# Performance work log

Hardware: AMD Instinct MI355X
Metric: run time of the kernel (lower is better)

## Reference

```python
import jax, jax.numpy as jnp
import numpy as np

N_LAYER = 4
N_HEAD = 8
N_EMBD = 512
HEAD_SIZE = N_EMBD // N_HEAD
VOCAB = 32000
BLOCK = 2048
WINDOW = 64
N_GLOBAL = 16
N_RANDOM = 16
B = 2
T = 2048


def setup_inputs() -> dict:
    key = jax.random.key(0)
    ks = jax.random.split(key, 24)
    s = 0.02
    inp = {
        "tok_emb": jax.random.normal(ks[0], (VOCAB, N_EMBD), jnp.float32) * s,
        "pos_emb": jax.random.normal(ks[1], (BLOCK, N_EMBD), jnp.float32) * s,
        "Wq": jax.random.normal(ks[2], (N_LAYER, N_HEAD, N_EMBD, HEAD_SIZE), jnp.float32) * s,
        "Wk": jax.random.normal(ks[3], (N_LAYER, N_HEAD, N_EMBD, HEAD_SIZE), jnp.float32) * s,
        "Wv": jax.random.normal(ks[4], (N_LAYER, N_HEAD, N_EMBD, HEAD_SIZE), jnp.float32) * s,
        "Wproj": jax.random.normal(ks[5], (N_LAYER, N_EMBD, N_EMBD), jnp.float32) * s,
        "bproj": jnp.zeros((N_LAYER, N_EMBD), jnp.float32),
        "ln1_g": jnp.ones((N_LAYER, N_EMBD), jnp.float32),
        "ln1_b": jnp.zeros((N_LAYER, N_EMBD), jnp.float32),
        "ln2_g": jnp.ones((N_LAYER, N_EMBD), jnp.float32),
        "ln2_b": jnp.zeros((N_LAYER, N_EMBD), jnp.float32),
        "W1": jax.random.normal(ks[6], (N_LAYER, N_EMBD, 4 * N_EMBD), jnp.float32) * s,
        "b1": jnp.zeros((N_LAYER, 4 * N_EMBD), jnp.float32),
        "W2": jax.random.normal(ks[7], (N_LAYER, 4 * N_EMBD, N_EMBD), jnp.float32) * s,
        "b2": jnp.zeros((N_LAYER, N_EMBD), jnp.float32),
        "lnf_g": jnp.ones((N_EMBD,), jnp.float32),
        "lnf_b": jnp.zeros((N_EMBD,), jnp.float32),
        "Wout": jax.random.normal(ks[8], (N_EMBD, VOCAB), jnp.float32) * s,
        "bout": jnp.zeros((VOCAB,), jnp.float32),
        "input_tokens": jax.random.randint(ks[9], (B, T), 0, VOCAB, jnp.int32),
        "random_cols": jax.random.randint(ks[10], (N_LAYER, N_HEAD, T, N_RANDOM), 0, T, jnp.int32),
    }
    return inp


def _layernorm(x, g, b):
    mu = jnp.mean(x, axis=-1, keepdims=True)
    var = jnp.var(x, axis=-1, keepdims=True)
    return (x - mu) * jax.lax.rsqrt(var + 1e-5) * g + b


def _static_masks(t):
    rows = jnp.arange(t)[:, None]
    cols = jnp.arange(t)[None, :]
    causal = rows >= cols
    local = (cols >= rows - WINDOW + 1) & (cols <= rows)
    glob = (rows < N_GLOBAL) | (cols < N_GLOBAL)
    return local | glob, causal  # base [T,T], causal [T,T]


def _random_mask(rc):  # rc: [H, T, R] -> [H, T, T] bool
    h, t, r = rc.shape
    m = jnp.zeros((h, t, t), dtype=bool)
    hi = jnp.arange(h)[:, None, None]
    ri = jnp.arange(t)[None, :, None]
    return m.at[hi, ri, rc].set(True)


def _forward(tok_emb, pos_emb, Wq, Wk, Wv, Wproj, bproj, ln1_g, ln1_b, ln2_g, ln2_b,
             W1, b1, W2, b2, lnf_g, lnf_b, Wout, bout, input_tokens, random_cols):
    b, t = input_tokens.shape
    x = tok_emb[input_tokens] + pos_emb[:t]  # [B,T,C]
    base, causal = _static_masks(t)
    scale = HEAD_SIZE ** -0.5
    neg_inf = jnp.finfo(x.dtype).min
    for l in range(N_LAYER):
        xn = _layernorm(x, ln1_g[l], ln1_b[l])
        q = jnp.einsum('btc,hcd->bhtd', xn, Wq[l])
        k = jnp.einsum('btc,hcd->bhtd', xn, Wk[l])
        v = jnp.einsum('btc,hcd->bhtd', xn, Wv[l])
        w = jnp.einsum('bhtd,bhsd->bhts', q, k) * scale  # [B,H,T,T]
        final = (base[None] | _random_mask(random_cols[l])) & causal[None]  # [H,T,T]
        w = jnp.where(final[None], w, neg_inf)
        w = jax.nn.softmax(w, axis=-1)
        attn = jnp.einsum('bhts,bhsd->bhtd', w, v)  # [B,H,T,hs]
        attn = attn.transpose(0, 2, 1, 3).reshape(b, t, N_EMBD)
        x = x + attn @ Wproj[l] + bproj[l]
        xn = _layernorm(x, ln2_g[l], ln2_b[l])
        h = jax.nn.relu(xn @ W1[l] + b1[l])
        x = x + h @ W2[l] + b2[l]
    x = _layernorm(x, lnf_g, lnf_b)
    return x @ Wout + bout  # logits [B,T,V]


def reference(tok_emb, pos_emb, Wq, Wk, Wv, Wproj, bproj, ln1_g, ln1_b, ln2_g, ln2_b,
              W1, b1, W2, b2, lnf_g, lnf_b, Wout, bout, input_tokens, random_cols):
    return _forward(tok_emb, pos_emb, Wq, Wk, Wv, Wproj, bproj, ln1_g, ln1_b, ln2_g, ln2_b,
                    W1, b1, W2, b2, lnf_g, lnf_b, Wout, bout, input_tokens, random_cols)
```

## Files before the change

### kernel.cpp

```cpp
#include <hip/hip_runtime.h>
#include <hip/hip_bf16.h>

#define NLAYER 4
#define NHEAD 8
#define CEMB 512
#define HS 64
#define VOCAB_N 32000
#define SEQT 2048
#define BATCH_N 2
#define MROWS (BATCH_N * SEQT)
#define WIN 64
#define NGLOB 16
#define NRAND 16
#define QB 16
#define VTW 104
#define PSW 104

typedef __attribute__((ext_vector_type(8))) __bf16 bf16x8;
typedef __attribute__((ext_vector_type(4))) float f32x4;
typedef __attribute__((ext_vector_type(8))) unsigned short u16x8;

__device__ __forceinline__ unsigned short f2bf(float f) {
    unsigned u = __float_as_uint(f);
    u += 0x7fffu + ((u >> 16) & 1u);
    return (unsigned short)(u >> 16);
}
__device__ __forceinline__ float bf2f(unsigned short v) {
    return __uint_as_float((unsigned)v << 16);
}

__device__ __forceinline__ void stage16(const unsigned short* g, unsigned short* l) {
    __builtin_amdgcn_global_load_lds(
        (const __attribute__((address_space(1))) void*)g,
        (__attribute__((address_space(3))) void*)l, 16, 0, 0);
}

__global__ __launch_bounds__(256) void transpose_all_kernel(
    const float* __restrict__ Wq, const float* __restrict__ Wk,
    const float* __restrict__ Wv, const float* __restrict__ Wproj,
    const float* __restrict__ W1, const float* __restrict__ W2,
    const float* __restrict__ Wout,
    unsigned short* __restrict__ wqkvT, unsigned short* __restrict__ wprojT,
    unsigned short* __restrict__ w1T, unsigned short* __restrict__ w2T,
    unsigned short* __restrict__ woutT)
{
    __shared__ float tle[64][65];
    const int bid = blockIdx.x;
    const float* src; unsigned short* dst; int Ks, Ns, k0, n0;
    if (bid < 768) {
        const int tile = bid & 7, rest = bid >> 3;
        const int l = rest / 24, r2 = rest % 24;
        const int sel = r2 >> 3, h = r2 & 7;
        const float* W = (sel == 0) ? Wq : (sel == 1) ? Wk : Wv;
        src = W + (size_t)(l * 8 + h) * 512 * 64;
        dst = wqkvT + ((size_t)l * 1536 + sel * 512 + h * 64) * 512;
        Ks = 512; Ns = 64; k0 = tile * 64; n0 = 0;
    } else if (bid < 1024) {
        const int idx = bid - 768, l = idx >> 6, t6 = idx & 63;
        src = Wproj + (size_t)l * 512 * 512;
        dst = wprojT + (size_t)l * 512 * 512;
        Ks = 512; Ns = 512; k0 = (t6 >> 3) * 64; n0 = (t6 & 7) * 64;
    } else if (bid < 2048) {
        const int idx = bid - 1024, l = idx >> 8, t8 = idx & 255;
        src = W1 + (size_t)l * 512 * 2048;
        dst = w1T + (size_t)l * 2048 * 512;
        Ks = 512; Ns = 2048; k0 = (t8 >> 5) * 64; n0 = (t8 & 31) * 64;
    } else if (bid < 3072) {
        const int idx = bid - 2048, l = idx >> 8, t8 = idx & 255;
        src = W2 + (size_t)l * 2048 * 512;
        dst = w2T + (size_t)l * 512 * 2048;
        Ks = 2048; Ns = 512; k0 = (t8 >> 3) * 64; n0 = (t8 & 7) * 64;
    } else {
        const int idx = bid - 3072;
        src = Wout; dst = woutT;
        Ks = 512; Ns = 32000; k0 = (idx / 500) * 64; n0 = (idx % 500) * 64;
    }
    const int tid = threadIdx.x;
    #pragma unroll
    for (int i = 0; i < 16; ++i) {
        const int idx = tid + i * 256;
        const int r = idx >> 6, c = idx & 63;
        tle[r][c] = src[(size_t)(k0 + r) * Ns + n0 + c];
    }
    __syncthreads();
    #pragma unroll
    for (int i = 0; i < 16; ++i) {
        const int idx = tid + i * 256;
        const int c = idx >> 6, r = idx & 63;
        dst[(size_t)(n0 + c) * Ks + k0 + r] = f2bf(tle[r][c]);
    }
}

__global__ __launch_bounds__(256) void embed_kernel(
    const float* __restrict__ tok_emb, const float* __restrict__ pos_emb,
    const int* __restrict__ toks, float* __restrict__ x)
{
    int i = blockIdx.x * 256 + threadIdx.x;
    int m = i >> 7;
    int c = (i & 127) << 2;
    int tok = toks[m];
    const float4 a = *(const float4*)&tok_emb[(size_t)tok * CEMB + c];
    const float4 p = *(const float4*)&pos_emb[(size_t)(m & (SEQT - 1)) * CEMB + c];
    float4 o;
    o.x = a.x + p.x; o.y = a.y + p.y; o.z = a.z + p.z; o.w = a.w + p.w;
    *(float4*)&x[(size_t)m * CEMB + c] = o;
}

__global__ __launch_bounds__(256) void ln_kernel(
    const float* __restrict__ x, const float* __restrict__ g,
    const float* __restrict__ b, unsigned short* __restrict__ out)
{
    const int wave = threadIdx.x >> 6, lane = threadIdx.x & 63;
    const int m = blockIdx.x * 4 + wave;
    const float* row = x + (size_t)m * CEMB;
    const float4 v0 = *(const float4*)&row[lane * 8];
    const float4 v1 = *(const float4*)&row[lane * 8 + 4];
    float s  = v0.x + v0.y + v0.z + v0.w + v1.x + v1.y + v1.z + v1.w;
    float s2 = v0.x*v0.x + v0.y*v0.y + v0.z*v0.z + v0.w*v0.w
             + v1.x*v1.x + v1.y*v1.y + v1.z*v1.z + v1.w*v1.w;
    #pragma unroll
    for (int off = 32; off > 0; off >>= 1) {
        s  += __shfl_xor(s, off);
        s2 += __shfl_xor(s2, off);
    }
    const float mu  = s * (1.f / CEMB);
    const float var = s2 * (1.f / CEMB) - mu * mu;
    const float rs  = rsqrtf(var + 1e-5f);
    const float vals[8] = {v0.x, v0.y, v0.z, v0.w, v1.x, v1.y, v1.z, v1.w};
    u16x8 o;
    #pragma unroll
    for (int j = 0; j < 8; ++j)
        o[j] = f2bf((vals[j] - mu) * rs * g[lane * 8 + j] + b[lane * 8 + j]);
    *(u16x8*)&out[(size_t)m * CEMB + lane * 8] = o;
}

template<int MODE, int NF>
__global__ __launch_bounds__(256) void gemm_kernel(
    const unsigned short* __restrict__ A, const unsigned short* __restrict__ Bt,
    const float* __restrict__ bias, const float* resid, void* outp,
    int M, int N, int K)
{
    __shared__ unsigned short sa[3][128 * 32];
    __shared__ unsigned short sb[3][NF * 32 * 32];
    const int tid = threadIdx.x;
    const int lane = tid & 63;
    const int wave = tid >> 6;
    const int wr = wave >> 1, wc = wave & 1;
    const int m0 = blockIdx.y * 128;
    const int n0 = blockIdx.x * (NF * 32);

    const int c0a = (wave * 2) * 64 + lane;
    const int c1a = (wave * 2 + 1) * 64 + lane;
    const int r0 = c0a >> 2, kk0 = (((c0a & 3) ^ ((r0 >> 1) & 3)) * 8);
    const int r1 = c1a >> 2, kk1 = (((c1a & 3) ^ ((r1 >> 1) & 3)) * 8);
    const unsigned short* ga0 = A + (size_t)(m0 + r0) * K + kk0;
    const unsigned short* ga1 = A + (size_t)(m0 + r1) * K + kk1;
    const int o0 = (wave * 2) * 512;
    const int o1 = (wave * 2 + 1) * 512;
    const int cb0 = (NF == 4) ? c0a : wave * 64 + lane;
    const int cb1 = c1a;
    const int rb0 = cb0 >> 2, kb0 = (((cb0 & 3) ^ ((rb0 >> 1) & 3)) * 8);
    const int rb1 = cb1 >> 2, kb1 = (((cb1 & 3) ^ ((rb1 >> 1) & 3)) * 8);
    const unsigned short* gb0 = Bt + (size_t)(n0 + rb0) * K + kb0;
    const unsigned short* gb1 = Bt + (size_t)(n0 + rb1) * K + kb1;
    const int ob0 = (NF == 4) ? o0 : wave * 512;
    const int ob1 = o1;

    f32x4 acc[4][NF] = {};
    const int lq = lane >> 4;
    const int fr = lane & 15;

    auto STAGE = [&](int tile, int buf) {
        const int kk = tile << 5;
        stage16(ga0 + kk, &sa[buf][o0]);
        stage16(ga1 + kk, &sa[buf][o1]);
        stage16(gb0 + kk, &sb[buf][ob0]);
        if constexpr (NF == 4) stage16(gb1 + kk, &sb[buf][ob1]);
    };

    const int nt = K >> 5;
    STAGE(0, 0);
    STAGE(1, 1);

    int cur = 0;
    for (int t = 0; t < nt; ++t) {
        if (t + 1 < nt) {
            if constexpr (NF == 2) asm volatile("s_waitcnt vmcnt(3)" ::: "memory");
            else                   asm volatile("s_waitcnt vmcnt(4)" ::: "memory");
        } else {
            asm volatile("s_waitcnt vmcnt(0)" ::: "memory");
        }
        __builtin_amdgcn_s_barrier();
        __builtin_amdgcn_sched_barrier(0);

        if (t + 2 < nt) {
            int b2 = cur + 2; if (b2 >= 3) b2 -= 3;
            STAGE(t + 2, b2);
        }

        bf16x8 af[4], bfr[NF];
        #pragma unroll
        for (int i = 0; i < 4; ++i) {
            const int Ra = wr * 64 + i * 16 + fr;
            af[i] = *reinterpret_cast<const bf16x8*>(
                &sa[cur][Ra * 32 + (((lq ^ ((Ra >> 1) & 3))) << 3)]);
        }
        #pragma unroll
        for (int i = 0; i < NF; ++i) {
            const int Rb = wc * (NF * 16) + i * 16 + fr;
            bfr[i] = *reinterpret_cast<const bf16x8*>(
                &sb[cur][Rb * 32 + (((lq ^ ((Rb >> 1) & 3))) << 3)]);
        }
        #pragma unroll
        for (int mi = 0; mi < 4; ++mi)
            #pragma unroll
            for (int ni = 0; ni < NF; ++ni)
                acc[mi][ni] = __builtin_amdgcn_mfma_f32_16x16x32_bf16(af[mi], bfr[ni], acc[mi][ni], 0, 0, 0);

        cur = (cur == 2) ? 0 : cur + 1;
    }

    #pragma unroll
    for (int mi = 0; mi < 4; ++mi) {
        #pragma unroll
        for (int ni = 0; ni < NF; ++ni) {
            const int gc = n0 + wc * (NF * 16) + ni * 16 + fr;
            const float bv = (MODE != 0) ? bias[gc] : 0.f;
            #pragma unroll
            for (int r = 0; r < 4; ++r) {
                const int gr = m0 + wr * 64 + mi * 16 + lq * 4 + r;
                float v = acc[mi][ni][r] + bv;
                if (MODE == 1) v += resid[(size_t)gr * N + gc];
                if (MODE == 2) v = fmaxf(v, 0.f);
                if (MODE == 0 || MODE == 2) {
                    ((unsigned short*)outp)[(size_t)gr * N + gc] = f2bf(v);
                } else {
                    ((float*)outp)[(size_t)gr * N + gc] = v;
                }
            }
        }
    }
}

__global__ __launch_bounds__(512) void gemm_logits_kernel(
    const unsigned short* __restrict__ A, const unsigned short* __restrict__ Bt,
    const float* __restrict__ bias, float* __restrict__ outp,
    int M, int N, int K)
{
    __shared__ unsigned short sa[2][256 * 32];
    __shared__ unsigned short sb[2][128 * 32];
    const int tid = threadIdx.x;
    const int lane = tid & 63;
    const int wave = tid >> 6;
    const int wr = wave >> 1, wc = wave & 1;

    const int flat = blockIdx.y * gridDim.x + blockIdx.x;
    const int q = (gridDim.x * gridDim.y) >> 3;
    const int nl = (flat & 7) * q + (flat >> 3);
    const int by = nl & 15;
    const int bx = nl >> 4;
    const int m0 = by * 256;
    const int n0 = bx * 128;

    const int c0a = (wave * 2) * 64 + lane;
    const int c1a = (wave * 2 + 1) * 64 + lane;
    const int r0 = c0a >> 2, kk0 = (((c0a & 3) ^ ((r0 >> 1) & 3)) * 8);
    const int r1 = c1a >> 2, kk1 = (((c1a & 3) ^ ((r1 >> 1) & 3)) * 8);
    const unsigned short* ga0 = A + (size_t)(m0 + r0) * K + kk0;
    const unsigned short* ga1 = A + (size_t)(m0 + r1) * K + kk1;
    const int o0 = (wave * 2) * 512;
    const int o1 = (wave * 2 + 1) * 512;
    const int cb0 = wave * 64 + lane;
    const int rb0 = cb0 >> 2, kb0 = (((cb0 & 3) ^ ((rb0 >> 1) & 3)) * 8);
    const unsigned short* gb0 = Bt + (size_t)(n0 + rb0) * K + kb0;
    const int ob0 = wave * 512;

    f32x4 acc[4][4] = {};
    const int lq = lane >> 4;
    const int fr = lane & 15;

    auto STAGE = [&](int t, int buf) {
        const int kk = t << 5;
        stage16(ga0 + kk, &sa[buf][o0]);
        stage16(ga1 + kk, &sa[buf][o1]);
        stage16(gb0 + kk, &sb[buf][ob0]);
    };

    const int nt = K >> 5;
    STAGE(0, 0);
    __syncthreads();
    int cur = 0;
    for (int t = 0; t < nt; ++t) {
        if (t + 1 < nt) STAGE(t + 1, cur ^ 1);
        bf16x8 af[4], bfr[4];
        #pragma unroll
        for (int i = 0; i < 4; ++i) {
            const int Ra = wr * 64 + i * 16 + fr;
            af[i] = *reinterpret_cast<const bf16x8*>(
                &sa[cur][Ra * 32 + (((lq ^ ((Ra >> 1) & 3))) << 3)]);
        }
        #pragma unroll
        for (int i = 0; i < 4; ++i) {
            const int Rb = wc * 64 + i * 16 + fr;
            bfr[i] = *reinterpret_cast<const bf16x8*>(
                &sb[cur][Rb * 32 + (((lq ^ ((Rb >> 1) & 3))) << 3)]);
        }
        #pragma unroll
        for (int mi = 0; mi < 4; ++mi)
            #pragma unroll
            for (int ni = 0; ni < 4; ++ni)
                acc[mi][ni] = __builtin_amdgcn_mfma_f32_16x16x32_bf16(af[mi], bfr[ni], acc[mi][ni], 0, 0, 0);
        __syncthreads();
        cur ^= 1;
    }

    #pragma unroll
    for (int mi = 0; mi < 4; ++mi) {
        #pragma unroll
        for (int ni = 0; ni < 4; ++ni) {
            const int gc = n0 + wc * 64 + ni * 16 + fr;
            const float bv = bias[gc];
            #pragma unroll
            for (int r = 0; r < 4; ++r) {
                const int gr = m0 + wr * 64 + mi * 16 + lq * 4 + r;
                outp[(size_t)gr * N + gc] = acc[mi][ni][r] + bv;
            }
        }
    }
}

__global__ __launch_bounds__(256) void attn_kernel(
    const unsigned short* __restrict__ qkv, const int* __restrict__ rc,
    unsigned short* __restrict__ attnout)
{
    __shared__ unsigned short Kw[80 * 64];
    __shared__ unsigned short Vt[64 * VTW];
    __shared__ unsigned short Ps[16 * PSW];
    __shared__ float rWs[16][40];
    __shared__ short rCs[16][40];
    __shared__ int   nBs[16];
    __shared__ float qinv[16];

    const int tid = threadIdx.x;
    const int wave = tid >> 6, lane = tid & 63;
    const int lq = lane >> 4, fr = lane & 15;
    const int bid = blockIdx.x;
    const int tb = bid & 127;
    const int h = (bid >> 7) & 7;
    const int b = bid >> 10;
    const int t0 = tb * QB;
    const int base = t0 - 63;

    const unsigned short* kb = qkv + (size_t)b * SEQT * 1536 + 512 + h * 64;
    const unsigned short* vb = qkv + (size_t)b * SEQT * 1536 + 1024 + h * 64;

    for (int c = tid; c < 79 * 8; c += 256) {
        const int r = c >> 3, j = c & 7;
        const int col = base + r;
        u16x8 kv = {0, 0, 0, 0, 0, 0, 0, 0};
        u16x8 vv = {0, 0, 0, 0, 0, 0, 0, 0};
        if (col >= 0) {
            kv = *(const u16x8*)&kb[(size_t)col * 1536 + j * 8];
            vv = *(const u16x8*)&vb[(size_t)col * 1536 + j * 8];
        }
        *(u16x8*)&Kw[r * 64 + ((j ^ (r & 7)) * 8)] = kv;
        #pragma unroll
        for (int e = 0; e < 8; ++e)
            Vt[(j * 8 + e) * VTW + r] = vv[e];
    }
    for (int i = tid; i < 64 * 17; i += 256) {
        const int d = i / 17, s = 79 + (i - d * 17);
        Vt[d * VTW + s] = 0;
    }
    __syncthreads();

    for (int u = 0; u < 4; ++u) {
        const int Q = wave * 4 + u;
        const int t = t0 + Q;
        const int m = b * SEQT + t;

        u16x8 qreg[8];
        #pragma unroll
        for (int j = 0; j < 8; ++j)
            qreg[j] = *(const u16x8*)&qkv[(size_t)m * 1536 + h * 64 + j * 8];

        const int row = Q + lane;
        const int colA = base + row;
        float sA;
        {
            float s = 0.f;
            #pragma unroll
            for (int j = 0; j < 8; ++j) {
                const u16x8 kc = *(const u16x8*)&Kw[row * 64 + ((j ^ (row & 7)) * 8)];
                #pragma unroll
                for (int e = 0; e < 8; ++e)
                    s += bf2f(kc[e]) * bf2f(qreg[j][e]);
            }
            sA = (colA >= NGLOB) ? s * 0.125f : -1e30f;
        }

        int colB = 0;
        bool vB = false;
        if (lane < NGLOB) {
            colB = lane;
            vB = (lane <= t);
        } else if (lane < 32) {
            colB = rc[((size_t)h * SEQT + t) * NRAND + (lane - 16)];
            vB = (colB >= NGLOB) && (colB <= t - WIN);
        }
        #pragma unroll
        for (int j = 0; j < 15; ++j) {
            const int cj = __shfl(colB, 16 + j);
            if (lane >= 16 && lane < 32 && (lane - 16) > j && cj == colB) vB = false;
        }

        float sB = -1e30f;
        if (vB) {
            float s = 0.f;
            const unsigned short* kr = &kb[(size_t)colB * 1536];
            #pragma unroll
            for (int j = 0; j < 8; ++j) {
                const u16x8 kc = *(const u16x8*)&kr[j * 8];
                #pragma unroll
                for (int e = 0; e < 8; ++e)
                    s += bf2f(kc[e]) * bf2f(qreg[j][e]);
            }
            sB = s * 0.125f;
        }

        float mx = fmaxf(sA, sB);
        #pragma unroll
        for (int off = 32; off > 0; off >>= 1) mx = fmaxf(mx, __shfl_xor(mx, off));
        const float e0 = (colA >= NGLOB) ? __expf(sA - mx) : 0.f;
        const float e1 = vB ? __expf(sB - mx) : 0.f;
        float sum = e0 + e1;
        #pragma unroll
        for (int off = 32; off > 0; off >>= 1) sum += __shfl_xor(sum, off);

        Ps[Q * PSW + Q + lane] = f2bf(e0);
        if (lane < 32) Ps[Q * PSW + ((Q + 64 + lane) % 96)] = 0;

        const unsigned long long bm = __ballot(vB);
        const int nB = __popcll(bm);
        const int pos = __popcll(bm & ((1ull << lane) - 1ull));
        if (vB) { rCs[Q][pos] = (short)colB; rWs[Q][pos] = e1; }
        if (lane >= 32 && lane < 36) {
            const int p = nB + (lane - 32);
            rCs[Q][p] = 0; rWs[Q][p] = 0.f;
        }
        if (lane == 0) { nBs[Q] = nB; qinv[Q] = 1.f / sum; }
    }
    __syncthreads();

    const int dmine = wave * 16 + fr;
    f32x4 of = {0.f, 0.f, 0.f, 0.f};
    #pragma unroll
    for (int ks = 0; ks < 3; ++ks) {
        const int s0 = ks * 32 + lq * 8;
        const bf16x8 ap = *reinterpret_cast<const bf16x8*>(&Ps[fr * PSW + s0]);
        const bf16x8 bv = *reinterpret_cast<const bf16x8*>(&Vt[dmine * VTW + s0]);
        of = __builtin_amdgcn_mfma_f32_16x16x32_bf16(ap, bv, of, 0, 0, 0);
    }

    #pragma unroll
    for (int r = 0; r < 4; ++r) {
        const int q2 = lq * 4 + r;
        float acc = of[r];
        const int nb4 = (nBs[q2] + 3) & ~3;
        for (int i = 0; i < nb4; i += 4) {
            const float w0 = rWs[q2][i + 0], w1 = rWs[q2][i + 1];
            const float w2 = rWs[q2][i + 2], w3 = rWs[q2][i + 3];
            const int   c0 = rCs[q2][i + 0], c1 = rCs[q2][i + 1];
            const int   c2 = rCs[q2][i + 2], c3 = rCs[q2][i + 3];
            acc += w0 * bf2f(vb[(size_t)c0 * 1536 + dmine])
                 + w1 * bf2f(vb[(size_t)c1 * 1536 + dmine])
                 + w2 * bf2f(vb[(size_t)c2 * 1536 + dmine])
                 + w3 * bf2f(vb[(size_t)c3 * 1536 + dmine]);
        }
        attnout[(size_t)(b * SEQT + t0 + q2) * CEMB + h * 64 + dmine] = f2bf(acc * qinv[q2]);
    }
}

extern "C" void kernel_launch(void* const* d_in, const int* in_sizes, int n_in,
                              void* d_out, int out_size, void* d_ws, size_t ws_size,
                              hipStream_t stream)
{
    const float* tok_emb = (const float*)d_in[0];
    const float* pos_emb = (const float*)d_in[1];
    const float* Wq    = (const float*)d_in[2];
    const float* Wk    = (const float*)d_in[3];
    const float* Wv    = (const float*)d_in[4];
    const float* Wproj = (const float*)d_in[5];
    const float* bproj = (const float*)d_in[6];
    const float* ln1g  = (const float*)d_in[7];
    const float* ln1b  = (const float*)d_in[8];
    const float* ln2g  = (const float*)d_in[9];
    const float* ln2b  = (const float*)d_in[10];
    const float* W1    = (const float*)d_in[11];
    const float* b1    = (const float*)d_in[12];
    const float* W2    = (const float*)d_in[13];
    const float* b2    = (const float*)d_in[14];
    const float* lnfg  = (const float*)d_in[15];
    const float* lnfb  = (const float*)d_in[16];
    const float* Wout  = (const float*)d_in[17];
    const float* bout  = (const float*)d_in[18];
    const int*   toks  = (const int*)d_in[19];
    const int*   rcols = (const int*)d_in[20];
    (void)in_sizes; (void)n_in; (void)out_size; (void)ws_size;

    char* ws = (char*)d_ws;
    size_t off = 0;
    auto ALLOC = [&](size_t bytes) -> void* {
        void* p = ws + off;
        off += (bytes + 255) & ~(size_t)255;
        return p;
    };
    float*          x      = (float*)ALLOC((size_t)MROWS * CEMB * 4);
    unsigned short* xnbf   = (unsigned short*)ALLOC((size_t)MROWS * CEMB * 2);
    unsigned short* qkv    = (unsigned short*)ALLOC((size_t)MROWS * 1536 * 2);
    unsigned short* attnbf = (unsigned short*)ALLOC((size_t)MROWS * CEMB * 2);
    unsigned short* hbf    = (unsigned short*)ALLOC((size_t)MROWS * 2048 * 2);
    unsigned short* wqkvT  = (unsigned short*)ALLOC((size_t)NLAYER * 1536 * 512 * 2);
    unsigned short* wprojT = (unsigned short*)ALLOC((size_t)NLAYER * 512 * 512 * 2);
    unsigned short* w1T    = (unsigned short*)ALLOC((size_t)NLAYER * 2048 * 512 * 2);
    unsigned short* w2T    = (unsigned short*)ALLOC((size_t)NLAYER * 512 * 2048 * 2);
    unsigned short* woutT  = (unsigned short*)ALLOC((size_t)VOCAB_N * 512 * 2);

    transpose_all_kernel<<<7072, 256, 0, stream>>>(
        Wq, Wk, Wv, Wproj, W1, W2, Wout, wqkvT, wprojT, w1T, w2T, woutT);

    embed_kernel<<<2048, 256, 0, stream>>>(tok_emb, pos_emb, toks, x);

    for (int l = 0; l < NLAYER; ++l) {
        ln_kernel<<<1024, 256, 0, stream>>>(x, ln1g + l * CEMB, ln1b + l * CEMB, xnbf);
        gemm_kernel<0, 2><<<dim3(24, 32), 256, 0, stream>>>(
            xnbf, wqkvT + (size_t)l * 1536 * 512, nullptr, nullptr, qkv, MROWS, 1536, 512);
        attn_kernel<<<2048, 256, 0, stream>>>(qkv, rcols + (size_t)l * NHEAD * SEQT * NRAND, attnbf);
        gemm_kernel<1, 2><<<dim3(8, 32), 256, 0, stream>>>(
            attnbf, wprojT + (size_t)l * 512 * 512, bproj + l * CEMB, x, x, MROWS, 512, 512);
        ln_kernel<<<1024, 256, 0, stream>>>(x, ln2g + l * CEMB, ln2b + l * CEMB, xnbf);
        gemm_kernel<2, 4><<<dim3(16, 32), 256, 0, stream>>>(
            xnbf, w1T + (size_t)l * 2048 * 512, b1 + l * 2048, nullptr, hbf, MROWS, 2048, 512);
        gemm_kernel<1, 2><<<dim3(8, 32), 256, 0, stream>>>(
            hbf, w2T + (size_t)l * 512 * 2048, b2 + l * CEMB, x, x, MROWS, 512, 2048);
    }
    ln_kernel<<<1024, 256, 0, stream>>>(x, lnfg, lnfb, xnbf);
    gemm_logits_kernel<<<dim3(250, 16), 512, 0, stream>>>(
        xnbf, woutT, bout, (float*)d_out, MROWS, VOCAB_N, 512);
}
```

Before: 1.013 ms.

## Retile logits GEMM to 128x256 and prefetch two stages ahead

```diff
diff --git a/kernel.cpp b/kernel.cpp
--- a/kernel.cpp
+++ b/kernel.cpp
@@ -247,70 +247,96 @@
     const float* __restrict__ bias, float* __restrict__ outp,
     int M, int N, int K)
 {
-    __shared__ unsigned short sa[2][256 * 32];
-    __shared__ unsigned short sb[2][128 * 32];
+    __shared__ unsigned short sa[2][128 * 32];
+    __shared__ unsigned short sb[2][256 * 32];
     const int tid = threadIdx.x;
     const int lane = tid & 63;
     const int wave = tid >> 6;
-    const int wr = wave >> 1, wc = wave & 1;
+    const int wr = wave >> 2, wc = wave & 3;
+    const int lq = lane >> 4, fr = lane & 15;
 
     const int flat = blockIdx.y * gridDim.x + blockIdx.x;
     const int q = (gridDim.x * gridDim.y) >> 3;
     const int nl = (flat & 7) * q + (flat >> 3);
-    const int by = nl & 15;
-    const int bx = nl >> 4;
-    const int m0 = by * 256;
-    const int n0 = bx * 128;
-
-    const int c0a = (wave * 2) * 64 + lane;
-    const int c1a = (wave * 2 + 1) * 64 + lane;
-    const int r0 = c0a >> 2, kk0 = (((c0a & 3) ^ ((r0 >> 1) & 3)) * 8);
-    const int r1 = c1a >> 2, kk1 = (((c1a & 3) ^ ((r1 >> 1) & 3)) * 8);
-    const unsigned short* ga0 = A + (size_t)(m0 + r0) * K + kk0;
-    const unsigned short* ga1 = A + (size_t)(m0 + r1) * K + kk1;
-    const int o0 = (wave * 2) * 512;
-    const int o1 = (wave * 2 + 1) * 512;
-    const int cb0 = wave * 64 + lane;
-    const int rb0 = cb0 >> 2, kb0 = (((cb0 & 3) ^ ((rb0 >> 1) & 3)) * 8);
-    const unsigned short* gb0 = Bt + (size_t)(n0 + rb0) * K + kb0;
-    const int ob0 = wave * 512;
+    const int by = nl & 31;
+    const int bx = nl >> 5;
+    const int m0 = by * 128;
+    const int n0 = bx * 256;
+
+    const int cB0 = tid,      rB0 = cB0 >> 2, kB0 = (((cB0 & 3) ^ ((rB0 >> 1) & 3)) * 8);
+    const int cB1 = tid + 512, rB1 = cB1 >> 2, kB1 = (((cB1 & 3) ^ ((rB1 >> 1) & 3)) * 8);
+    const unsigned short* gb0 = Bt + (size_t)(n0 + rB0) * K + kB0;
+    const unsigned short* gb1 = Bt + (size_t)(n0 + rB1) * K + kB1;
+    const int cA = tid, rA = cA >> 2, kA = (((cA & 3) ^ ((rA >> 1) & 3)) * 8);
+    const unsigned short* ga = A + (size_t)(m0 + rA) * K + kA;
+
+    unsigned short* const sb0d[2] = { &sb[0][(size_t)wave * 512], &sb[1][(size_t)wave * 512] };
+    unsigned short* const sb1d[2] = { &sb[0][(size_t)wave * 512 + 4096], &sb[1][(size_t)wave * 512 + 4096] };
+    unsigned short* const sad[2]  = { &sa[0][(size_t)wave * 512], &sa[1][(size_t)wave * 512] };
 
     f32x4 acc[4][4] = {};
-    const int lq = lane >> 4;
-    const int fr = lane & 15;
 
     auto STAGE = [&](int t, int buf) {
         const int kk = t << 5;
-        stage16(ga0 + kk, &sa[buf][o0]);
-        stage16(ga1 + kk, &sa[buf][o1]);
-        stage16(gb0 + kk, &sb[buf][ob0]);
+        stage16(gb0 + kk, sb0d[buf]);
+        stage16(gb1 + kk, sb1d[buf]);
+        stage16(ga + kk,  sad[buf]);
     };
 
     const int nt = K >> 5;
     STAGE(0, 0);
-    __syncthreads();
+    STAGE(1, 1);
+
     int cur = 0;
     for (int t = 0; t < nt; ++t) {
-        if (t + 1 < nt) STAGE(t + 1, cur ^ 1);
-        bf16x8 af[4], bfr[4];
-        #pragma unroll
-        for (int i = 0; i < 4; ++i) {
+        if (t + 1 < nt) {
+            asm volatile("s_waitcnt vmcnt(3)" ::: "memory");
+        } else {
+            asm volatile("s_waitcnt vmcnt(0)" ::: "memory");
+        }
+        __builtin_amdgcn_s_barrier();
+        __builtin_amdgcn_sched_barrier(0);
+
+        bf16x8 bfr[4], afA[2], afB[2];
+        #pragma unroll
+        for (int j = 0; j < 4; ++j) {
+            const int Rb = wc * 64 + j * 16 + fr;
+            bfr[j] = *reinterpret_cast<const bf16x8*>(
+                &sb[cur][Rb * 32 + ((lq ^ ((Rb >> 1) & 3)) << 3)]);
+        }
+        #pragma unroll
+        for (int i = 0; i < 2; ++i) {
             const int Ra = wr * 64 + i * 16 + fr;
-            af[i] = *reinterpret_cast<const bf16x8*>(
-                &sa[cur][Ra * 32 + (((lq ^ ((Ra >> 1) & 3))) << 3)]);
-        }
-        #pragma unroll
-        for (int i = 0; i < 4; ++i) {
-            const int Rb = wc * 64 + i * 16 + fr;
-            bfr[i] = *reinterpret_cast<const bf16x8*>(
-                &sb[cur][Rb * 32 + (((lq ^ ((Rb >> 1) & 3))) << 3)]);
-        }
-        #pragma unroll
-        for (int mi = 0; mi < 4; ++mi)
+            afA[i] = *reinterpret_cast<const bf16x8*>(
+                &sa[cur][Ra * 32 + ((lq ^ ((Ra >> 1) & 3)) << 3)]);
+        }
+        __builtin_amdgcn_s_setprio(1);
+        #pragma unroll
+        for (int mi = 0; mi < 2; ++mi)
             #pragma unroll
             for (int ni = 0; ni < 4; ++ni)
-                acc[mi][ni] = __builtin_amdgcn_mfma_f32_16x16x32_bf16(af[mi], bfr[ni], acc[mi][ni], 0, 0, 0);
-        __syncthreads();
+                acc[mi][ni] = __builtin_amdgcn_mfma_f32_16x16x32_bf16(afA[mi], bfr[ni], acc[mi][ni], 0, 0, 0);
+        __builtin_amdgcn_s_setprio(0);
+        __builtin_amdgcn_s_barrier();
+        __builtin_amdgcn_sched_barrier(0);
+
+        #pragma unroll
+        for (int i = 0; i < 2; ++i) {
+            const int Ra = wr * 64 + (2 + i) * 16 + fr;
+            afB[i] = *reinterpret_cast<const bf16x8*>(
+                &sa[cur][Ra * 32 + ((lq ^ ((Ra >> 1) & 3)) << 3)]);
+        }
+        __builtin_amdgcn_s_setprio(1);
+        #pragma unroll
+        for (int mi = 0; mi < 2; ++mi)
+            #pragma unroll
+            for (int ni = 0; ni < 4; ++ni)
+                acc[2 + mi][ni] = __builtin_amdgcn_mfma_f32_16x16x32_bf16(afB[mi], bfr[ni], acc[2 + mi][ni], 0, 0, 0);
+        __builtin_amdgcn_s_setprio(0);
+        __builtin_amdgcn_s_barrier();
+        __builtin_amdgcn_sched_barrier(0);
+
+        if (t + 2 < nt) STAGE(t + 2, cur);
         cur ^= 1;
     }
 
@@ -545,6 +571,6 @@
             hbf, w2T + (size_t)l * 512 * 2048, b2 + l * CEMB, x, x, MROWS, 512, 2048);
     }
     ln_kernel<<<1024, 256, 0, stream>>>(x, lnfg, lnfb, xnbf);
-    gemm_logits_kernel<<<dim3(250, 16), 512, 0, stream>>>(
+    gemm_logits_kernel<<<dim3(125, 32), 512, 0, stream>>>(
         xnbf, woutT, bout, (float*)d_out, MROWS, VOCAB_N, 512);
 }
```

Result: no change. 1.023 ms (+1.0%).
